# Optimization experiments

Measured on AMD Instinct MI355X. Metric: run time of the kernel, lower is better.

The kernel has to match this reference:

```python
import jax, jax.numpy as jnp
import numpy as np

BN_EPS = 1e-5


def setup_inputs() -> dict:
    key = jax.random.key(0)
    ks = jax.random.split(key, 8)
    B, C, N = 2, 64, 8192
    s = 1.0 / np.sqrt(C)
    return {
        "feature": jax.random.normal(ks[0], (B, C, N, 1), dtype=jnp.float32),
        "wa": jax.random.normal(ks[1], (C, C), dtype=jnp.float32) * s,
        "ba": jnp.zeros((C,), jnp.float32),
        "wb": jax.random.normal(ks[2], (C, C), dtype=jnp.float32) * s,
        "bb": jnp.zeros((C,), jnp.float32),
        "wm": jax.random.normal(ks[3], (C, C), dtype=jnp.float32) * s,
        "bm": jnp.zeros((C,), jnp.float32),
        "bn_gamma": jnp.ones((C,), jnp.float32),
        "bn_beta": jnp.zeros((C,), jnp.float32),
        "bn_mean": jax.random.normal(ks[4], (C,), dtype=jnp.float32) * 0.1,
        "bn_var": jnp.ones((C,), jnp.float32) + jax.random.uniform(ks[5], (C,), dtype=jnp.float32),
        "alpha": jnp.array(0.5, jnp.float32),
    }


def _pam(feature, wa, ba, wb, bb, wm, bm, g, bt, mean, var, alpha):
    # feature: [B, C, N, 1]
    x = feature[..., 0]  # [B, C, N]
    a = jnp.einsum('oc,bcn->bon', wa, x) + ba[None, :, None]  # fc_a, 1x1 conv
    b = jnp.einsum('oc,bcn->bon', wb, x) + bb[None, :, None]  # fc_b
    # att = a^T b : [B, N, N], softmax over last dim (dim=2)
    att = jax.nn.softmax(jnp.einsum('bcn,bcm->bnm', a, b), axis=2)
    # mlp branch: 1x1 conv + inference BatchNorm
    m = jnp.einsum('oc,bcn->bon', wm, x) + bm[None, :, None]
    m = (m - mean[None, :, None]) * jax.lax.rsqrt(var + BN_EPS)[None, :, None]
    m = m * g[None, :, None] + bt[None, :, None]
    # (att @ m^T)^T : out[b,c,n] = sum_m att[b,n,m] * m[b,c,m]
    out = jnp.einsum('bnm,bcm->bcn', att, m)
    return feature + alpha * out[..., None]


def reference(feature, wa, ba, wb, bb, wm, bm, bn_gamma, bn_beta, bn_mean, bn_var, alpha):
    # GFA calls self.pam twice (fam is unused in its forward): f1 + f2 == 2 * pam(feature)
    p = _pam(feature, wa, ba, wb, bb, wm, bm, bn_gamma, bn_beta, bn_mean, bn_var, alpha)
    return p + p
```

## Files before the change

kernel.cpp:

```cpp
#include <hip/hip_runtime.h>
#include <hip/hip_bf16.h>
#include <math.h>

#define CDIM 64
#define BATCH 2
#define KSPLIT 8
#define TK 64
#define M_FIX 44.0f
#define LOG2E 1.44269504f

typedef __bf16 bf16x8 __attribute__((ext_vector_type(8)));
typedef __bf16 bf16x4 __attribute__((ext_vector_type(4)));
typedef float f32x4 __attribute__((ext_vector_type(4)));

__global__ __launch_bounds__(256) void gfa_stage1(
    const float* __restrict__ feature,
    const float* __restrict__ wa, const float* __restrict__ ba,
    const float* __restrict__ wb, const float* __restrict__ bb,
    const float* __restrict__ wm, const float* __restrict__ bm,
    const float* __restrict__ gma, const float* __restrict__ bta,
    const float* __restrict__ mean, const float* __restrict__ var,
    __bf16* __restrict__ Q, __bf16* __restrict__ K, __bf16* __restrict__ V,
    int N)
{
    const int tid  = threadIdx.x;
    const int w    = tid >> 6;
    const int lane = tid & 63;
    const int l15  = lane & 15;
    const int quad = lane >> 4;
    const int n0    = blockIdx.x * 64;
    const int which = blockIdx.y;
    const int b     = blockIdx.z;

    __shared__ __align__(16) char s1lds[35328];
    float*  Xs  = (float*)s1lds;
    __bf16* Whi = (__bf16*)(s1lds + 16896);
    __bf16* Wlo = (__bf16*)(s1lds + 26112);
    __bf16* Ts  = (__bf16*)s1lds;

    const float* wsel = (which == 0) ? wa : (which == 1) ? wb : wm;
    const float* bsel = (which == 0) ? ba : (which == 1) ? bb : bm;
    const float wscale = (which == 1) ? LOG2E : 1.0f;

    const float* fb = feature + (size_t)b * CDIM * N;
#pragma unroll
    for (int p = 0; p < 4; p++) {
        int idx = p * 256 + tid;
        int c = idx >> 4, n4 = (idx & 15) << 2;
        float4 v = *(const float4*)&fb[(size_t)c * N + n0 + n4];
        *(float2*)&Xs[c * 66 + n4]     = make_float2(v.x, v.y);
        *(float2*)&Xs[c * 66 + n4 + 2] = make_float2(v.z, v.w);
    }
#pragma unroll
    for (int p = 0; p < 4; p++) {
        int idx = p * 256 + tid;
        int o = idx >> 4, c4 = (idx & 15) << 2;
        float4 v = *(const float4*)&wsel[o * 64 + c4];
        bf16x4 hi, lo;
        float vv[4] = {v.x * wscale, v.y * wscale, v.z * wscale, v.w * wscale};
#pragma unroll
        for (int r = 0; r < 4; r++) {
            hi[r] = (__bf16)vv[r];
            lo[r] = (__bf16)(vv[r] - (float)hi[r]);
        }
        *(bf16x4*)&Whi[o * 72 + c4] = hi;
        *(bf16x4*)&Wlo[o * 72 + c4] = lo;
    }
    __syncthreads();

    const int nb = w * 16;
    bf16x8 xh[2], xl[2];
#pragma unroll
    for (int kc = 0; kc < 2; kc++) {
#pragma unroll
        for (int j = 0; j < 8; j++) {
            float xv = Xs[(kc * 32 + quad * 8 + j) * 66 + nb + l15];
            __bf16 h = (__bf16)xv;
            xh[kc][j] = h;
            xl[kc][j] = (__bf16)(xv - (float)h);
        }
    }

    f32x4 acc[4];
#pragma unroll
    for (int ot = 0; ot < 4; ot++) acc[ot] = (f32x4){0.f, 0.f, 0.f, 0.f};

#pragma unroll
    for (int ot = 0; ot < 4; ot++) {
#pragma unroll
        for (int kc = 0; kc < 2; kc++) {
            bf16x8 wh = *(const bf16x8*)&Whi[(ot * 16 + l15) * 72 + kc * 32 + quad * 8];
            bf16x8 wl = *(const bf16x8*)&Wlo[(ot * 16 + l15) * 72 + kc * 32 + quad * 8];
            acc[ot] = __builtin_amdgcn_mfma_f32_16x16x32_bf16(wh, xh[kc], acc[ot], 0, 0, 0);
            acc[ot] = __builtin_amdgcn_mfma_f32_16x16x32_bf16(wl, xh[kc], acc[ot], 0, 0, 0);
            acc[ot] = __builtin_amdgcn_mfma_f32_16x16x32_bf16(wh, xl[kc], acc[ot], 0, 0, 0);
        }
    }

    __syncthreads();
    if (which < 2) {
        __bf16* O = (which == 0 ? Q : K) + (size_t)b * N * CDIM;
#pragma unroll
        for (int ot = 0; ot < 4; ot++) {
            int o0 = ot * 16 + quad * 4;
            float4 b4 = *(const float4*)&bsel[o0];
            float bv[4] = {b4.x * wscale, b4.y * wscale, b4.z * wscale, b4.w * wscale};
            bf16x4 pk;
#pragma unroll
            for (int r = 0; r < 4; r++) pk[r] = (__bf16)(acc[ot][r] + bv[r]);
            *(bf16x4*)&Ts[(nb + l15) * 68 + o0] = pk;
        }
        __syncthreads();
#pragma unroll
        for (int p = 0; p < 2; p++) {
            int idx = p * 256 + tid;
            int row = idx >> 3, c8 = (idx & 7) * 8;
            *(int4*)&O[(size_t)(n0 + row) * CDIM + c8] = *(int4*)&Ts[row * 68 + c8];
        }
    } else {
        __bf16* Vb = V + (size_t)b * CDIM * N;
#pragma unroll
        for (int ot = 0; ot < 4; ot++) {
            int o0 = ot * 16 + quad * 4;
            float4 b4 = *(const float4*)&bsel[o0];
            float4 m4 = *(const float4*)&mean[o0];
            float4 v4 = *(const float4*)&var[o0];
            float4 g4 = *(const float4*)&gma[o0];
            float4 t4 = *(const float4*)&bta[o0];
            float bv[4] = {b4.x, b4.y, b4.z, b4.w};
            float mv[4] = {m4.x, m4.y, m4.z, m4.w};
            float vv[4] = {v4.x, v4.y, v4.z, v4.w};
            float gv[4] = {g4.x, g4.y, g4.z, g4.w};
            float tv[4] = {t4.x, t4.y, t4.z, t4.w};
#pragma unroll
            for (int r = 0; r < 4; r++) {
                float s = gv[r] * rsqrtf(vv[r] + 1e-5f);
                float val = (acc[ot][r] + bv[r] - mv[r]) * s + tv[r];
                Ts[(o0 + r) * 68 + nb + l15] = (__bf16)val;
            }
        }
        __syncthreads();
#pragma unroll
        for (int p = 0; p < 2; p++) {
            int idx = p * 256 + tid;
            int row = idx >> 3, n8 = (idx & 7) * 8;
            *(int4*)&Vb[(size_t)row * N + n0 + n8] = *(int4*)&Ts[row * 68 + n8];
        }
    }
}

__global__ __launch_bounds__(256, 4) void gfa_stage2(
    const __bf16* __restrict__ Q, const __bf16* __restrict__ K,
    const __bf16* __restrict__ V,
    float* __restrict__ Upart, float* __restrict__ stats, int N)
{
    const int tid  = threadIdx.x;
    const int w    = tid >> 6;
    const int lane = tid & 63;
    const int l15  = lane & 15;
    const int quad = lane >> 4;
    const int qt   = blockIdx.x;
    const int sp   = blockIdx.y;
    const int b    = blockIdx.z;
    const int qb0  = qt * 128 + w * 32;
    const int QT   = N >> 6;

    __shared__ __align__(16) char lds[36864];
    char* Kt = lds;
    char* Vt = lds + 9216;
    char* Pw = lds + 18432 + w * 4608;

    const __bf16* Qg = Q + (size_t)b * N * CDIM;
    const __bf16* Kg = K + (size_t)b * N * CDIM;
    const __bf16* Vg = V + (size_t)b * CDIM * N;
    const int kvb = sp * (N / KSPLIT);
    const int r8 = tid >> 3, c16 = (tid & 7) * 16;

    bf16x8 qf[2][2];
#pragma unroll
    for (int nt = 0; nt < 2; nt++)
#pragma unroll
        for (int kc = 0; kc < 2; kc++)
            qf[nt][kc] = *(const bf16x8*)(Qg + (size_t)(qb0 + nt * 16 + l15) * CDIM + kc * 32 + quad * 8);

    f32x4 acc[2][4];
#pragma unroll
    for (int nt = 0; nt < 2; nt++)
#pragma unroll
        for (int tc = 0; tc < 4; tc++) acc[nt][tc] = (f32x4){0.f, 0.f, 0.f, 0.f};
    float l_run[2] = {0.f, 0.f};

    const int NIT = N / KSPLIT / TK;
    for (int it = 0; it < NIT; it++) {
        const int kv0 = kvb + it * TK;
        __syncthreads();
#pragma unroll
        for (int p = 0; p < 2; p++) {
            int r = p * 32 + r8;
            *(int4*)(Kt + r * 144 + c16) =
                *(const int4*)((const char*)Kg + (size_t)(kv0 + r) * 128 + c16);
        }
#pragma unroll
        for (int p = 0; p < 2; p++) {
            int r = p * 32 + r8;
            *(int4*)(Vt + r * 144 + c16) =
                *(const int4*)((const char*)Vg + ((size_t)r * N + kv0) * 2 + c16);
        }
        __syncthreads();

#pragma unroll
        for (int nt = 0; nt < 2; nt++) {
            f32x4 lt[4];
#pragma unroll
            for (int t = 0; t < 4; t++) {
                f32x4 a = (f32x4){0.f, 0.f, 0.f, 0.f};
#pragma unroll
                for (int kc = 0; kc < 2; kc++) {
                    bf16x8 kf = *(const bf16x8*)(Kt + (16 * t + l15) * 144 + kc * 64 + quad * 16);
                    a = __builtin_amdgcn_mfma_f32_16x16x32_bf16(kf, qf[nt][kc], a, 0, 0, 0);
                }
                lt[t] = a;
            }
            float s = 0.f;
#pragma unroll
            for (int t = 0; t < 4; t++) {
                bf16x4 pb;
#pragma unroll
                for (int r = 0; r < 4; r++) {
                    float p = __builtin_amdgcn_exp2f(lt[t][r] - M_FIX);
                    s += p;
                    pb[r] = (__bf16)p;
                }
                *(bf16x4*)(Pw + nt * 2304 + l15 * 144 + (16 * t + quad * 4) * 2) = pb;
            }
            s += __shfl_xor(s, 16);
            s += __shfl_xor(s, 32);
            l_run[nt] += s;
        }

#pragma unroll
        for (int ks = 0; ks < 2; ks++) {
            bf16x8 pf0 = *(const bf16x8*)(Pw + 0    + l15 * 144 + ks * 64 + quad * 16);
            bf16x8 pf1 = *(const bf16x8*)(Pw + 2304 + l15 * 144 + ks * 64 + quad * 16);
#pragma unroll
            for (int tc = 0; tc < 4; tc++) {
                bf16x8 vf = *(const bf16x8*)(Vt + (16 * tc + l15) * 144 + ks * 64 + quad * 16);
                acc[0][tc] = __builtin_amdgcn_mfma_f32_16x16x32_bf16(vf, pf0, acc[0][tc], 0, 0, 0);
                acc[1][tc] = __builtin_amdgcn_mfma_f32_16x16x32_bf16(vf, pf1, acc[1][tc], 0, 0, 0);
            }
        }
    }

    const int qt64 = qt * 2 + (w >> 1);
    float* Ub = Upart + ((size_t)(b * KSPLIT + sp) * QT + qt64) * 4096;
    float* Sb = stats + ((size_t)(b * KSPLIT + sp) * QT + qt64) * 64;
#pragma unroll
    for (int nt = 0; nt < 2; nt++) {
        int qq = (w & 1) * 32 + nt * 16 + l15;
#pragma unroll
        for (int tc = 0; tc < 4; tc++)
#pragma unroll
            for (int r = 0; r < 4; r++) {
                int c = tc * 16 + quad * 4 + r;
                Ub[c * 64 + qq] = acc[nt][tc][r];
            }
        if (quad == 0) Sb[qq] = l_run[nt];
    }
}

__global__ __launch_bounds__(256) void gfa_reduce(
    const float* __restrict__ feature, const float* __restrict__ alpha_p,
    const float* __restrict__ Upart, const float* __restrict__ stats,
    float* __restrict__ out, int N)
{
    const int qt = blockIdx.x;
    const int cq = blockIdx.y;
    const int b  = blockIdx.z;
    const int q  = threadIdx.x & 63;
    const int c0 = cq * 16 + (threadIdx.x >> 6) * 4;
    const int QT = N >> 6;

    float L = 0.f;
#pragma unroll
    for (int s = 0; s < KSPLIT; s++)
        L += stats[((size_t)(b * KSPLIT + s) * QT + qt) * 64 + q];

    float u[4] = {0.f, 0.f, 0.f, 0.f};
#pragma unroll
    for (int s = 0; s < KSPLIT; s++) {
        const float* Ub = Upart + ((size_t)(b * KSPLIT + s) * QT + qt) * 4096;
#pragma unroll
        for (int i = 0; i < 4; i++)
            u[i] += Ub[(c0 + i) * 64 + q];
    }

    float scale = 2.f * alpha_p[0] / L;
    const int n = qt * 64 + q;
#pragma unroll
    for (int i = 0; i < 4; i++) {
        size_t gi = ((size_t)b * CDIM + c0 + i) * N + n;
        out[gi] = 2.f * feature[gi] + scale * u[i];
    }
}

extern "C" void kernel_launch(void* const* d_in, const int* in_sizes, int n_in,
                              void* d_out, int out_size, void* d_ws, size_t ws_size,
                              hipStream_t stream) {
    const float* feature = (const float*)d_in[0];
    const float* wa   = (const float*)d_in[1];
    const float* ba   = (const float*)d_in[2];
    const float* wb   = (const float*)d_in[3];
    const float* bb   = (const float*)d_in[4];
    const float* wm   = (const float*)d_in[5];
    const float* bm   = (const float*)d_in[6];
    const float* gma  = (const float*)d_in[7];
    const float* bta  = (const float*)d_in[8];
    const float* mean = (const float*)d_in[9];
    const float* var  = (const float*)d_in[10];
    const float* alpha = (const float*)d_in[11];
    const int N = in_sizes[0] / (BATCH * CDIM);

    __bf16* Q = (__bf16*)d_ws;
    __bf16* K = Q + (size_t)BATCH * N * CDIM;
    __bf16* V = K + (size_t)BATCH * N * CDIM;
    float* Upart = (float*)(V + (size_t)BATCH * N * CDIM);
    float* stats = Upart + (size_t)BATCH * KSPLIT * (N / 64) * 4096;

    dim3 g1(N / 64, 3, BATCH);
    gfa_stage1<<<g1, 256, 0, stream>>>(feature, wa, ba, wb, bb, wm, bm,
                                       gma, bta, mean, var, Q, K, V, N);
    dim3 g2(N / 128, KSPLIT, BATCH);
    gfa_stage2<<<g2, 256, 0, stream>>>(Q, K, V, Upart, stats, N);
    dim3 g3(N / 64, 4, BATCH);
    gfa_reduce<<<g3, 256, 0, stream>>>(feature, alpha, Upart, stats, (float*)d_out, N);
}
```

Before: 140.2 us.

## Switch attention stage to 32x32 MFMA tiles with 64 queries per wave and bf16 partials

Rewrites the flash-style attention stage so each wave handles 64 queries with 32x32x16 bf16 MFMA instead of 16x16x32, doubling the queries per block and halving the grid. The aim is to reuse each K/V tile loaded into LDS across more queries and to issue fewer, larger matrix instructions. The split-K partial outputs are now stored in bf16 rather than fp32, which halves the partial-sum write and read traffic in the reduce kernel but lowers precision. LDS per block grows and occupancy hints drop from 4 to 2 blocks per CU.

```diff
diff --git a/kernel.cpp b/kernel.cpp
--- a/kernel.cpp
+++ b/kernel.cpp
@@ -12,6 +12,7 @@
 typedef __bf16 bf16x8 __attribute__((ext_vector_type(8)));
 typedef __bf16 bf16x4 __attribute__((ext_vector_type(4)));
 typedef float f32x4 __attribute__((ext_vector_type(4)));
+typedef float f32x16 __attribute__((ext_vector_type(16)));
 
 __global__ __launch_bounds__(256) void gfa_stage1(
     const float* __restrict__ feature,
@@ -149,26 +150,26 @@
     }
 }
 
-__global__ __launch_bounds__(256, 4) void gfa_stage2(
+__global__ __launch_bounds__(256, 2) void gfa_stage2(
     const __bf16* __restrict__ Q, const __bf16* __restrict__ K,
     const __bf16* __restrict__ V,
-    float* __restrict__ Upart, float* __restrict__ stats, int N)
+    __bf16* __restrict__ Upart, float* __restrict__ stats, int N)
 {
     const int tid  = threadIdx.x;
     const int w    = tid >> 6;
     const int lane = tid & 63;
-    const int l15  = lane & 15;
-    const int quad = lane >> 4;
-    const int qt   = blockIdx.x;
+    const int l31  = lane & 31;
+    const int half = lane >> 5;
+    const int qt_  = blockIdx.x;
     const int sp   = blockIdx.y;
     const int b    = blockIdx.z;
-    const int qb0  = qt * 128 + w * 32;
+    const int qb   = qt_ * 256 + w * 64;
     const int QT   = N >> 6;
 
-    __shared__ __align__(16) char lds[36864];
+    __shared__ __align__(16) char lds[55296];
     char* Kt = lds;
     char* Vt = lds + 9216;
-    char* Pw = lds + 18432 + w * 4608;
+    char* Pw = lds + 18432 + w * 9216;
 
     const __bf16* Qg = Q + (size_t)b * N * CDIM;
     const __bf16* Kg = K + (size_t)b * N * CDIM;
@@ -176,18 +177,21 @@
     const int kvb = sp * (N / KSPLIT);
     const int r8 = tid >> 3, c16 = (tid & 7) * 16;
 
-    bf16x8 qf[2][2];
-#pragma unroll
-    for (int nt = 0; nt < 2; nt++)
-#pragma unroll
-        for (int kc = 0; kc < 2; kc++)
-            qf[nt][kc] = *(const bf16x8*)(Qg + (size_t)(qb0 + nt * 16 + l15) * CDIM + kc * 32 + quad * 8);
-
-    f32x4 acc[2][4];
-#pragma unroll
-    for (int nt = 0; nt < 2; nt++)
-#pragma unroll
-        for (int tc = 0; tc < 4; tc++) acc[nt][tc] = (f32x4){0.f, 0.f, 0.f, 0.f};
+    bf16x8 qf[2][4];
+#pragma unroll
+    for (int qt = 0; qt < 2; qt++)
+#pragma unroll
+        for (int kc = 0; kc < 4; kc++)
+            qf[qt][kc] = *(const bf16x8*)((const char*)Qg
+                + (size_t)(qb + qt * 32 + l31) * 128 + kc * 32 + half * 16);
+
+    f32x16 acc[2][2];
+#pragma unroll
+    for (int qt = 0; qt < 2; qt++)
+#pragma unroll
+        for (int ct = 0; ct < 2; ct++)
+#pragma unroll
+            for (int r = 0; r < 16; r++) acc[qt][ct][r] = 0.f;
     float l_run[2] = {0.f, 0.f};
 
     const int NIT = N / KSPLIT / TK;
@@ -209,68 +213,74 @@
         __syncthreads();
 
 #pragma unroll
-        for (int nt = 0; nt < 2; nt++) {
-            f32x4 lt[4];
-#pragma unroll
-            for (int t = 0; t < 4; t++) {
-                f32x4 a = (f32x4){0.f, 0.f, 0.f, 0.f};
-#pragma unroll
-                for (int kc = 0; kc < 2; kc++) {
-                    bf16x8 kf = *(const bf16x8*)(Kt + (16 * t + l15) * 144 + kc * 64 + quad * 16);
-                    a = __builtin_amdgcn_mfma_f32_16x16x32_bf16(kf, qf[nt][kc], a, 0, 0, 0);
+        for (int kvt = 0; kvt < 2; kvt++) {
+            bf16x8 kf[4];
+#pragma unroll
+            for (int kc = 0; kc < 4; kc++)
+                kf[kc] = *(const bf16x8*)(Kt + (kvt * 32 + l31) * 144 + kc * 32 + half * 16);
+#pragma unroll
+            for (int qt = 0; qt < 2; qt++) {
+                f32x16 s16;
+#pragma unroll
+                for (int r = 0; r < 16; r++) s16[r] = 0.f;
+#pragma unroll
+                for (int kc = 0; kc < 4; kc++)
+                    s16 = __builtin_amdgcn_mfma_f32_32x32x16_bf16(kf[kc], qf[qt][kc], s16, 0, 0, 0);
+                float s = 0.f;
+#pragma unroll
+                for (int rg = 0; rg < 4; rg++) {
+                    bf16x4 pb;
+#pragma unroll
+                    for (int r = 0; r < 4; r++) {
+                        float p = __builtin_amdgcn_exp2f(s16[rg * 4 + r] - M_FIX);
+                        s += p;
+                        pb[r] = (__bf16)p;
+                    }
+                    *(bf16x4*)(Pw + (qt * 32 + l31) * 144
+                               + (kvt * 32 + rg * 8 + half * 4) * 2) = pb;
                 }
-                lt[t] = a;
+                l_run[qt] += s;
             }
-            float s = 0.f;
-#pragma unroll
-            for (int t = 0; t < 4; t++) {
-                bf16x4 pb;
-#pragma unroll
-                for (int r = 0; r < 4; r++) {
-                    float p = __builtin_amdgcn_exp2f(lt[t][r] - M_FIX);
-                    s += p;
-                    pb[r] = (__bf16)p;
-                }
-                *(bf16x4*)(Pw + nt * 2304 + l15 * 144 + (16 * t + quad * 4) * 2) = pb;
+        }
+
+#pragma unroll
+        for (int ks = 0; ks < 4; ks++) {
+            bf16x8 vf[2], pf[2];
+#pragma unroll
+            for (int ct = 0; ct < 2; ct++)
+                vf[ct] = *(const bf16x8*)(Vt + (ct * 32 + l31) * 144 + ks * 32 + half * 16);
+#pragma unroll
+            for (int qt = 0; qt < 2; qt++)
+                pf[qt] = *(const bf16x8*)(Pw + (qt * 32 + l31) * 144 + ks * 32 + half * 16);
+#pragma unroll
+            for (int qt = 0; qt < 2; qt++)
+#pragma unroll
+                for (int ct = 0; ct < 2; ct++)
+                    acc[qt][ct] = __builtin_amdgcn_mfma_f32_32x32x16_bf16(vf[ct], pf[qt], acc[qt][ct], 0, 0, 0);
+        }
+    }
+
+    const int qt64 = qt_ * 4 + w;
+    __bf16* Ub = Upart + ((size_t)(b * KSPLIT + sp) * QT + qt64) * 4096;
+    float*  Sb = stats + ((size_t)(b * KSPLIT + sp) * QT + qt64) * 64;
+#pragma unroll
+    for (int qt = 0; qt < 2; qt++) {
+        float s = l_run[qt] + __shfl_xor(l_run[qt], 32);
+        int qq = qt * 32 + l31;
+#pragma unroll
+        for (int ct = 0; ct < 2; ct++)
+#pragma unroll
+            for (int r = 0; r < 16; r++) {
+                int c = ct * 32 + (r & 3) + 8 * (r >> 2) + 4 * half;
+                Ub[c * 64 + qq] = (__bf16)acc[qt][ct][r];
             }
-            s += __shfl_xor(s, 16);
-            s += __shfl_xor(s, 32);
-            l_run[nt] += s;
-        }
-
-#pragma unroll
-        for (int ks = 0; ks < 2; ks++) {
-            bf16x8 pf0 = *(const bf16x8*)(Pw + 0    + l15 * 144 + ks * 64 + quad * 16);
-            bf16x8 pf1 = *(const bf16x8*)(Pw + 2304 + l15 * 144 + ks * 64 + quad * 16);
-#pragma unroll
-            for (int tc = 0; tc < 4; tc++) {
-                bf16x8 vf = *(const bf16x8*)(Vt + (16 * tc + l15) * 144 + ks * 64 + quad * 16);
-                acc[0][tc] = __builtin_amdgcn_mfma_f32_16x16x32_bf16(vf, pf0, acc[0][tc], 0, 0, 0);
-                acc[1][tc] = __builtin_amdgcn_mfma_f32_16x16x32_bf16(vf, pf1, acc[1][tc], 0, 0, 0);
-            }
-        }
-    }
-
-    const int qt64 = qt * 2 + (w >> 1);
-    float* Ub = Upart + ((size_t)(b * KSPLIT + sp) * QT + qt64) * 4096;
-    float* Sb = stats + ((size_t)(b * KSPLIT + sp) * QT + qt64) * 64;
-#pragma unroll
-    for (int nt = 0; nt < 2; nt++) {
-        int qq = (w & 1) * 32 + nt * 16 + l15;
-#pragma unroll
-        for (int tc = 0; tc < 4; tc++)
-#pragma unroll
-            for (int r = 0; r < 4; r++) {
-                int c = tc * 16 + quad * 4 + r;
-                Ub[c * 64 + qq] = acc[nt][tc][r];
-            }
-        if (quad == 0) Sb[qq] = l_run[nt];
+        if (half == 0) Sb[qq] = s;
     }
 }
 
 __global__ __launch_bounds__(256) void gfa_reduce(
     const float* __restrict__ feature, const float* __restrict__ alpha_p,
-    const float* __restrict__ Upart, const float* __restrict__ stats,
+    const __bf16* __restrict__ Upart, const float* __restrict__ stats,
     float* __restrict__ out, int N)
 {
     const int qt = blockIdx.x;
@@ -288,10 +298,10 @@
     float u[4] = {0.f, 0.f, 0.f, 0.f};
 #pragma unroll
     for (int s = 0; s < KSPLIT; s++) {
-        const float* Ub = Upart + ((size_t)(b * KSPLIT + s) * QT + qt) * 4096;
+        const __bf16* Ub = Upart + ((size_t)(b * KSPLIT + s) * QT + qt) * 4096;
 #pragma unroll
         for (int i = 0; i < 4; i++)
-            u[i] += Ub[(c0 + i) * 64 + q];
+            u[i] += (float)Ub[(c0 + i) * 64 + q];
     }
 
     float scale = 2.f * alpha_p[0] / L;
@@ -323,13 +333,13 @@
     __bf16* Q = (__bf16*)d_ws;
     __bf16* K = Q + (size_t)BATCH * N * CDIM;
     __bf16* V = K + (size_t)BATCH * N * CDIM;
-    float* Upart = (float*)(V + (size_t)BATCH * N * CDIM);
-    float* stats = Upart + (size_t)BATCH * KSPLIT * (N / 64) * 4096;
+    __bf16* Upart = V + (size_t)BATCH * N * CDIM;
+    float* stats = (float*)(Upart + (size_t)BATCH * KSPLIT * (N / 64) * 4096);
 
     dim3 g1(N / 64, 3, BATCH);
     gfa_stage1<<<g1, 256, 0, stream>>>(feature, wa, ba, wb, bb, wm, bm,
                                        gma, bta, mean, var, Q, K, V, N);
-    dim3 g2(N / 128, KSPLIT, BATCH);
+    dim3 g2(N / 256, KSPLIT, BATCH);
     gfa_stage2<<<g2, 256, 0, stream>>>(Q, K, V, Upart, stats, N);
     dim3 g3(N / 64, 4, BATCH);
     gfa_reduce<<<g3, 256, 0, stream>>>(feature, alpha, Upart, stats, (float*)d_out, N);
```

Result: faster. 129.7 us (-7.5%).
